# Optimization experiments

Hardware: AMD Instinct MI355X
Metric: run time of the kernel (lower is better)

## Reference

```python
import jax, jax.numpy as jnp
import numpy as np

D_MODEL = 1024
N_HEADS = 16
HEAD_DIM = D_MODEL // N_HEADS
NEG = -10000.0  # module uses -10000, not -inf


def setup_inputs() -> dict:
    key = jax.random.key(0)
    ks = jax.random.split(key, 8)
    B, T = 4, 2048
    q = jax.random.normal(ks[0], (B, T, D_MODEL), dtype=jnp.float32)
    k = jax.random.normal(ks[1], (B, T, D_MODEL), dtype=jnp.float32)
    v = jax.random.normal(ks[2], (B, T, D_MODEL), dtype=jnp.float32)
    attn_mask = jnp.ones((B, T), dtype=jnp.float32)
    # xavier_uniform for square [d, d] weights: limit = sqrt(6/(d+d))
    lim = float(np.sqrt(6.0 / (D_MODEL + D_MODEL)))
    Wq = jax.random.uniform(ks[3], (D_MODEL, D_MODEL), jnp.float32, -lim, lim)
    Wk = jax.random.uniform(ks[4], (D_MODEL, D_MODEL), jnp.float32, -lim, lim)
    Wv = jax.random.uniform(ks[5], (D_MODEL, D_MODEL), jnp.float32, -lim, lim)
    Wo = jax.random.uniform(ks[6], (D_MODEL, D_MODEL), jnp.float32, -lim, lim)
    return {"q": q, "k": k, "v": v, "attn_mask": attn_mask,
            "Wq": Wq, "Wk": Wk, "Wv": Wv, "Wo": Wo, "mask_future": 1}


def _split_heads(x):
    B, T, _ = x.shape
    return x.reshape(B, T, N_HEADS, HEAD_DIM).transpose(0, 2, 1, 3)  # [B,H,T,D]


def reference(q, k, v, attn_mask, Wq, Wk, Wv, Wo, mask_future):
    # torch Linear: y = x @ W.T  (weights stored [out, in])
    qh = _split_heads(jnp.einsum('btd,ed->bte', q, Wq))
    kh = _split_heads(jnp.einsum('btd,ed->bte', k, Wk))
    vh = _split_heads(jnp.einsum('btd,ed->bte', v, Wv))
    L, S = qh.shape[-2], kh.shape[-2]
    # dual scale: each of q and k scaled by 1/d**0.25
    scale = 1.0 / jnp.sqrt(jnp.sqrt(jnp.float32(HEAD_DIM)))
    scores = jnp.einsum('bhld,bhsd->bhls', qh * scale, kh * scale)
    if mask_future:
        causal_bias = jnp.triu(jnp.full((L, S), NEG, dtype=scores.dtype), k=1)
        scores = scores + causal_bias
    # padding mask: attn_mask [B, S] -> broadcast [B,1,1,S]; 0 entries -> -10000
    pad = attn_mask[:, None, None, :]
    scores = jnp.where(pad == 0, jnp.asarray(NEG, scores.dtype), scores)
    probs = jax.nn.softmax(scores, axis=-1)  # dropout p=0.0 -> identity
    ctx = jnp.einsum('bhls,bhsd->bhld', probs, vh)
    B = ctx.shape[0]
    ctx = ctx.transpose(0, 2, 1, 3).reshape(B, L, D_MODEL)
    return jnp.einsum('btd,ed->bte', ctx, Wo)
```

## Files before the change

kernel.cpp:

```cpp
#include <hip/hip_runtime.h>

typedef unsigned short u16;
typedef __attribute__((ext_vector_type(8))) _Float16 f16x8;
typedef __attribute__((ext_vector_type(2))) __fp16 fp16v2;
typedef __attribute__((ext_vector_type(4))) float f32x4;
typedef __attribute__((ext_vector_type(16))) float f32x16;

#define T_SEQ 2048
#define NH 16
#define DH 64
#define DM 1024
#define NEG2 (-14426.95f)
#define QS2 (0.42466089f)

__device__ __forceinline__ unsigned pk2(float a, float b) {
  union { fp16v2 v; unsigned u; } c;
  c.v = __builtin_amdgcn_cvt_pkrtz(a, b);
  return c.u;
}
__device__ __forceinline__ u16 f2h(float a) {
  union { _Float16 h; u16 u; } c; c.h = (_Float16)a; return c.u;
}

__device__ __forceinline__ void async_load16(const void* g, void* l) {
  __builtin_amdgcn_global_load_lds(
      (const __attribute__((address_space(1))) unsigned int*)(g),
      (__attribute__((address_space(3))) unsigned int*)(l), 16, 0, 0);
}

__global__ __launch_bounds__(256) void convert_all(
    const float* __restrict__ q, const float* __restrict__ k, const float* __restrict__ v,
    const float* __restrict__ Wq, const float* __restrict__ Wk, const float* __restrict__ Wv,
    const float* __restrict__ Wo, u16* __restrict__ xb, u16* __restrict__ wb) {
  int blk = blockIdx.x;
  const float* src; u16* dst;
  if (blk < 12288) {
    int s = blk >> 12;
    src = (s == 0) ? q : (s == 1) ? k : v;
    dst = xb + (size_t)s * 8388608u;
    blk &= 4095;
  } else {
    int s = (blk - 12288) >> 9;
    src = (s == 0) ? Wq : (s == 1) ? Wk : (s == 2) ? Wv : Wo;
    dst = wb + (size_t)s * 1048576u;
    blk = (blk - 12288) & 511;
  }
  size_t base = (size_t)blk * 2048 + (size_t)threadIdx.x * 8;
  float4 a = *(const float4*)(src + base);
  float4 b2 = *(const float4*)(src + base + 4);
  uint4 st;
  st.x = pk2(a.x, a.y); st.y = pk2(a.z, a.w);
  st.z = pk2(b2.x, b2.y); st.w = pk2(b2.z, b2.w);
  *(uint4*)(dst + base) = st;
}

__global__ __launch_bounds__(512) void gemm_qkv(const u16* __restrict__ A,
                                                const u16* __restrict__ Wqb,
                                                const u16* __restrict__ Wkb,
                                                const u16* __restrict__ Wvb,
                                                u16* __restrict__ Qh, u16* __restrict__ Kh,
                                                u16* __restrict__ VTh) {
  __shared__ char lds[147456];
  const int tid = threadIdx.x;
  const int wid = tid >> 6, lane = tid & 63;
  const int l32 = lane & 31, lh = lane >> 5;
  const int m0 = blockIdx.x * 256;
  const int n0 = blockIdx.y * 128;
  const int which = n0 >> 10;
  const int n0l = n0 & 1023;
  const u16* As = A + (size_t)which * 8388608u;
  const u16* Bw = (which == 0) ? Wqb : (which == 1) ? Wkb : Wvb;
  f32x16 acc[2][2] = {};

  const u16* gsrc[6]; int ldso[6];
#pragma unroll
  for (int u = 0; u < 6; ++u) {
    int c = wid * 6 + u;
    ldso[u] = c * 1024;
    if (c < 32)
      gsrc[u] = As + (size_t)(m0 + (c >> 2) * 32 + l32) * 1024 + (c & 3) * 16 + lh * 8;
    else {
      int cw = c - 32;
      gsrc[u] = Bw + (size_t)(n0l + (cw >> 2) * 32 + l32) * 1024 + (cw & 3) * 16 + lh * 8;
    }
  }

  const int rOff = (which < 2) ? 32768 : 0;
  const int cOff = 32768 - rOff;
  const int rgo = (which < 2) ? ((wid & 1) * 2) : ((wid >> 1) * 2);
  const int cgo = (which < 2) ? ((wid >> 1) * 2) : ((wid & 1) * 2);

#pragma unroll
  for (int u = 0; u < 6; ++u) async_load16(gsrc[u] + 0 * 64, lds + 0 * 49152 + ldso[u]);
#pragma unroll
  for (int u = 0; u < 6; ++u) async_load16(gsrc[u] + 1 * 64, lds + 1 * 49152 + ldso[u]);
  asm volatile("s_waitcnt vmcnt(6)" ::: "memory");
  __builtin_amdgcn_s_barrier();
  asm volatile("" ::: "memory");

  int slotc = 0, slotn = 2;
  for (int kt = 0; kt < 16; ++kt) {
    char* bufc = lds + slotc * 49152;
    char* bufn = lds + slotn * 49152;
    const char* rb = bufc + rOff;
    const char* cb = bufc + cOff;
    f16x8 a0[4], a1[4], b0[4], b1[4];
#pragma unroll
    for (int k = 0; k < 4; ++k) {
      a0[k] = *(const f16x8*)(rb + ((rgo + 0) * 4 + k) * 1024 + lane * 16);
      b0[k] = *(const f16x8*)(cb + ((cgo + 0) * 4 + k) * 1024 + lane * 16);
      b1[k] = *(const f16x8*)(cb + ((cgo + 1) * 4 + k) * 1024 + lane * 16);
    }
    if (kt < 14) {
#pragma unroll
      for (int u = 0; u < 3; ++u) async_load16(gsrc[u] + (kt + 2) * 64, bufn + ldso[u]);
    }
    asm volatile("" ::: "memory");
    __builtin_amdgcn_s_barrier();
    asm volatile("s_waitcnt lgkmcnt(0)" ::: "memory");
    __builtin_amdgcn_sched_barrier(0);
    __builtin_amdgcn_s_setprio(1);
#pragma unroll
    for (int k = 0; k < 4; ++k) {
      acc[0][0] = __builtin_amdgcn_mfma_f32_32x32x16_f16(a0[k], b0[k], acc[0][0], 0, 0, 0);
      acc[0][1] = __builtin_amdgcn_mfma_f32_32x32x16_f16(a0[k], b1[k], acc[0][1], 0, 0, 0);
    }
    __builtin_amdgcn_s_setprio(0);
    asm volatile("" ::: "memory");
    __builtin_amdgcn_s_barrier();
#pragma unroll
    for (int k = 0; k < 4; ++k)
      a1[k] = *(const f16x8*)(rb + ((rgo + 1) * 4 + k) * 1024 + lane * 16);
    if (kt < 14) {
#pragma unroll
      for (int u = 3; u < 6; ++u) async_load16(gsrc[u] + (kt + 2) * 64, bufn + ldso[u]);
    }
    if (kt < 14) asm volatile("s_waitcnt vmcnt(6)" ::: "memory");
    else         asm volatile("s_waitcnt vmcnt(0)" ::: "memory");
    asm volatile("" ::: "memory");
    __builtin_amdgcn_s_barrier();
    asm volatile("s_waitcnt lgkmcnt(0)" ::: "memory");
    __builtin_amdgcn_sched_barrier(0);
    __builtin_amdgcn_s_setprio(1);
#pragma unroll
    for (int k = 0; k < 4; ++k) {
      acc[1][0] = __builtin_amdgcn_mfma_f32_32x32x16_f16(a1[k], b0[k], acc[1][0], 0, 0, 0);
      acc[1][1] = __builtin_amdgcn_mfma_f32_32x32x16_f16(a1[k], b1[k], acc[1][1], 0, 0, 0);
    }
    __builtin_amdgcn_s_setprio(0);
    asm volatile("" ::: "memory");
    __builtin_amdgcn_s_barrier();
    slotc = (slotc == 2) ? 0 : slotc + 1;
    slotn = (slotn == 2) ? 0 : slotn + 1;
  }

  const float s = (which < 2) ? QS2 : 1.0f;
  const int b = m0 >> 11, t0 = m0 & 2047, h0 = n0l >> 6;
  __syncthreads();
  if (which < 2) {
#pragma unroll
    for (int i = 0; i < 2; ++i)
#pragma unroll
      for (int j = 0; j < 2; ++j) {
        int colb = (wid >> 1) * 64 + j * 32 + l32;
        int rowb = (wid & 1) * 64 + i * 32 + 4 * lh;
#pragma unroll
        for (int g = 0; g < 4; ++g) {
          uint2 pv;
          pv.x = pk2(acc[i][j][4 * g + 0] * s, acc[i][j][4 * g + 1] * s);
          pv.y = pk2(acc[i][j][4 * g + 2] * s, acc[i][j][4 * g + 3] * s);
          *(uint2*)(lds + colb * 264 + (rowb + 8 * g) * 2) = pv;
        }
      }
    __syncthreads();
    u16* O = which ? Kh : Qh;
#pragma unroll
    for (int p = 0; p < 8; ++p) {
      int row = p * 32 + (tid >> 4);
      int seg = tid & 15;
      uint4 val = *(const uint4*)(lds + row * 264 + seg * 16);
      int hl = seg >> 3, dh0 = (seg & 7) * 8;
      *(uint4*)(O + (((size_t)(b * NH + h0 + hl) * T_SEQ + t0 + row) << 6) + dh0) = val;
    }
  } else {
#pragma unroll
    for (int i = 0; i < 2; ++i)
#pragma unroll
      for (int j = 0; j < 2; ++j) {
        int colb = (wid & 1) * 64 + j * 32 + l32;
        int rowb = (wid >> 1) * 64 + i * 32 + 4 * lh;
#pragma unroll
        for (int g = 0; g < 4; ++g) {
          uint2 pv;
          pv.x = pk2(acc[i][j][4 * g + 0], acc[i][j][4 * g + 1]);
          pv.y = pk2(acc[i][j][4 * g + 2], acc[i][j][4 * g + 3]);
          *(uint2*)(lds + colb * 520 + (rowb + 8 * g) * 2) = pv;
        }
      }
    __syncthreads();
#pragma unroll
    for (int p = 0; p < 8; ++p) {
      int row = p * 16 + (tid >> 5);
      int seg = tid & 31;
      uint4 val = *(const uint4*)(lds + row * 520 + seg * 16);
      int h = h0 + (row >> 6), dh = row & 63;
      *(uint4*)(VTh + (((size_t)(b * NH + h) * DH + dh) << 11) + t0 + seg * 8) = val;
    }
  }
}

__global__ __launch_bounds__(512) void gemm_out(const u16* __restrict__ A,
                                                const u16* __restrict__ Bw,
                                                float* __restrict__ O) {
  __shared__ char lds[147456];
  const int tid = threadIdx.x;
  const int wid = tid >> 6, lane = tid & 63;
  const int l32 = lane & 31, lh = lane >> 5;
  const int m0 = blockIdx.x * 256, n0 = blockIdx.y * 128;
  f32x16 acc[2][2] = {};

  const u16* gsrc[6]; int ldso[6];
#pragma unroll
  for (int u = 0; u < 6; ++u) {
    int c = wid * 6 + u;
    ldso[u] = c * 1024;
    if (c < 32)
      gsrc[u] = A + (size_t)(m0 + (c >> 2) * 32 + l32) * 1024 + (c & 3) * 16 + lh * 8;
    else {
      int cw = c - 32;
      gsrc[u] = Bw + (size_t)(n0 + (cw >> 2) * 32 + l32) * 1024 + (cw & 3) * 16 + lh * 8;
    }
  }
  const int rgo = (wid >> 1) * 2, cgo = (wid & 1) * 2;

#pragma unroll
  for (int u = 0; u < 6; ++u) async_load16(gsrc[u] + 0 * 64, lds + 0 * 49152 + ldso[u]);
#pragma unroll
  for (int u = 0; u < 6; ++u) async_load16(gsrc[u] + 1 * 64, lds + 1 * 49152 + ldso[u]);
  asm volatile("s_waitcnt vmcnt(6)" ::: "memory");
  __builtin_amdgcn_s_barrier();
  asm volatile("" ::: "memory");

  int slotc = 0, slotn = 2;
  for (int kt = 0; kt < 16; ++kt) {
    char* bufc = lds + slotc * 49152;
    char* bufn = lds + slotn * 49152;
    const char* rb = bufc;
    const char* cb = bufc + 32768;
    f16x8 a0[4], a1[4], b0[4], b1[4];
#pragma unroll
    for (int k = 0; k < 4; ++k) {
      a0[k] = *(const f16x8*)(rb + ((rgo + 0) * 4 + k) * 1024 + lane * 16);
      b0[k] = *(const f16x8*)(cb + ((cgo + 0) * 4 + k) * 1024 + lane * 16);
      b1[k] = *(const f16x8*)(cb + ((cgo + 1) * 4 + k) * 1024 + lane * 16);
    }
    if (kt < 14) {
#pragma unroll
      for (int u = 0; u < 3; ++u) async_load16(gsrc[u] + (kt + 2) * 64, bufn + ldso[u]);
    }
    asm volatile("" ::: "memory");
    __builtin_amdgcn_s_barrier();
    asm volatile("s_waitcnt lgkmcnt(0)" ::: "memory");
    __builtin_amdgcn_sched_barrier(0);
    __builtin_amdgcn_s_setprio(1);
#pragma unroll
    for (int k = 0; k < 4; ++k) {
      acc[0][0] = __builtin_amdgcn_mfma_f32_32x32x16_f16(a0[k], b0[k], acc[0][0], 0, 0, 0);
      acc[0][1] = __builtin_amdgcn_mfma_f32_32x32x16_f16(a0[k], b1[k], acc[0][1], 0, 0, 0);
    }
    __builtin_amdgcn_s_setprio(0);
    asm volatile("" ::: "memory");
    __builtin_amdgcn_s_barrier();
#pragma unroll
    for (int k = 0; k < 4; ++k)
      a1[k] = *(const f16x8*)(rb + ((rgo + 1) * 4 + k) * 1024 + lane * 16);
    if (kt < 14) {
#pragma unroll
      for (int u = 3; u < 6; ++u) async_load16(gsrc[u] + (kt + 2) * 64, bufn + ldso[u]);
    }
    if (kt < 14) asm volatile("s_waitcnt vmcnt(6)" ::: "memory");
    else         asm volatile("s_waitcnt vmcnt(0)" ::: "memory");
    asm volatile("" ::: "memory");
    __builtin_amdgcn_s_barrier();
    asm volatile("s_waitcnt lgkmcnt(0)" ::: "memory");
    __builtin_amdgcn_sched_barrier(0);
    __builtin_amdgcn_s_setprio(1);
#pragma unroll
    for (int k = 0; k < 4; ++k) {
      acc[1][0] = __builtin_amdgcn_mfma_f32_32x32x16_f16(a1[k], b0[k], acc[1][0], 0, 0, 0);
      acc[1][1] = __builtin_amdgcn_mfma_f32_32x32x16_f16(a1[k], b1[k], acc[1][1], 0, 0, 0);
    }
    __builtin_amdgcn_s_setprio(0);
    asm volatile("" ::: "memory");
    __builtin_amdgcn_s_barrier();
    slotc = (slotc == 2) ? 0 : slotc + 1;
    slotn = (slotn == 2) ? 0 : slotn + 1;
  }
#pragma unroll
  for (int i = 0; i < 2; ++i)
#pragma unroll
    for (int j = 0; j < 2; ++j) {
      int col = n0 + (wid & 1) * 64 + j * 32 + l32;
      int rowb = m0 + (wid >> 1) * 64 + i * 32 + 4 * lh;
#pragma unroll
      for (int g = 0; g < 4; ++g)
#pragma unroll
        for (int rr = 0; rr < 4; ++rr)
          O[(size_t)(rowb + 8 * g + rr) * 1024 + col] = acc[i][j][4 * g + rr];
    }
}

__global__ __launch_bounds__(512) void attn_kernel(const u16* __restrict__ Qh,
                                                   const u16* __restrict__ Kh,
                                                   const u16* __restrict__ VTh,
                                                   const float* __restrict__ attn_mask,
                                                   const int* __restrict__ mfp,
                                                   u16* __restrict__ ctx) {
  __shared__ char kls[2][8192];
  __shared__ char vls[2][8192];
  __shared__ char pls[8][2048];
  __shared__ int mzf;

  const int tid = threadIdx.x;
  const int wid = tid >> 6, lane = tid & 63;
  const int lm = lane & 15, lq = lane >> 4;
  const int bid = blockIdx.x;
  const int bh_i = bid & 63;
  const int qt = 15 - (bid >> 6);
  const int b = bh_i >> 4, h = bh_i & 15;
  const int mf = *mfp;
  const size_t bh = (size_t)(b * NH + h);
  const u16* Qbh = Qh + bh * T_SEQ * DH;
  const u16* Kbh = Kh + bh * T_SEQ * DH;
  const u16* VTbh = VTh + bh * DH * T_SEQ;
  const float* amb = attn_mask + (size_t)b * T_SEQ;

  f16x8 onev;
#pragma unroll
  for (int i = 0; i < 8; ++i) onev[i] = (_Float16)1.0f;

  if (tid == 0) mzf = 0;
  __syncthreads();
  {
    int az = 0;
    for (int i = tid; i < T_SEQ; i += 512) az |= (amb[i] == 0.0f);
    if (az) mzf = 1;
  }
  __syncthreads();
  const int maskzero = mzf;

  const int qw = qt * 128 + wid * 16;
  f16x8 qf[2];
  qf[0] = *(const f16x8*)(Qbh + (size_t)(qw + lm) * DH + lq * 8);
  qf[1] = *(const f16x8*)(Qbh + (size_t)(qw + lm) * DH + 32 + lq * 8);

  f32x4 acc[4] = {};
  f32x4 accs = {};
  float mprev = -1e30f;

  const int nch = mf ? (qt + 1) * 2 : 32;
  {
    async_load16(Kbh + (size_t)((wid >> 1) * 16 + lm) * DH + (wid & 1) * 32 + lq * 8,
                 kls[0] + wid * 1024);
    async_load16(VTbh + (size_t)((wid >> 1) * 16 + lm) * T_SEQ + (wid & 1) * 32 + lq * 8,
                 vls[0] + wid * 1024);
  }
  for (int c = 0; c < nch; ++c) {
    const int s0 = c * 64;
    asm volatile("s_waitcnt vmcnt(0)" ::: "memory");
    __builtin_amdgcn_s_barrier();
    asm volatile("" ::: "memory");
    if (c + 1 < nch) {
      const int s1 = s0 + 64;
      async_load16(Kbh + (size_t)(s1 + (wid >> 1) * 16 + lm) * DH + (wid & 1) * 32 + lq * 8,
                   kls[(c + 1) & 1] + wid * 1024);
      async_load16(VTbh + (size_t)((wid >> 1) * 16 + lm) * T_SEQ + s1 + (wid & 1) * 32 + lq * 8,
                   vls[(c + 1) & 1] + wid * 1024);
    }
    const char* kcur = kls[c & 1];
    const char* vcur = vls[c & 1];

    f32x4 sc[4];
    for (int st = 0; st < 4; ++st) {
      f32x4 z = {0.f, 0.f, 0.f, 0.f};
      sc[st] = z;
      for (int kk = 0; kk < 2; ++kk) {
        f16x8 kf = *(const f16x8*)(kcur + ((st * 2 + kk) * 64 + lane) * 16);
        sc[st] = __builtin_amdgcn_mfma_f32_16x16x32_f16(kf, qf[kk], sc[st], 0, 0, 0);
      }
    }
    if (maskzero) {
      for (int st = 0; st < 4; ++st) {
        f32x4 mb = *(const f32x4*)(amb + s0 + st * 16 + lq * 4);
        for (int r = 0; r < 4; ++r)
          if (mb[r] == 0.0f) sc[st][r] += NEG2;
      }
    }
    if (mf && (s0 + 64 > qw)) {
      int qg = qw + lm;
      for (int st = 0; st < 4; ++st)
        for (int r = 0; r < 4; ++r)
          if (s0 + st * 16 + lq * 4 + r > qg) sc[st][r] = NEG2;
    }
    float u0 = fmaxf(fmaxf(sc[0][0], sc[0][1]), sc[0][2]);
    float u1 = fmaxf(fmaxf(sc[0][3], sc[1][0]), sc[1][1]);
    float u2 = fmaxf(fmaxf(sc[1][2], sc[1][3]), sc[2][0]);
    float u3 = fmaxf(fmaxf(sc[2][1], sc[2][2]), sc[2][3]);
    float u4 = fmaxf(fmaxf(sc[3][0], sc[3][1]), sc[3][2]);
    float mx = fmaxf(fmaxf(fmaxf(u0, u1), u2), fmaxf(fmaxf(u3, u4), sc[3][3]));
    mx = fmaxf(mx, __shfl_xor(mx, 16));
    mx = fmaxf(mx, __shfl_xor(mx, 32));
    if (__ballot(mx > mprev + 8.0f) != 0ull) {
      float mn2 = fmaxf(mprev, mx);
      float alpha = exp2f(mprev - mn2);
      for (int r = 0; r < 4; ++r) {
        float ar = __shfl(alpha, lq * 4 + r);
        for (int nt = 0; nt < 4; ++nt) acc[nt][r] *= ar;
        accs[r] *= ar;
      }
      mprev = mn2;
    }
    for (int st = 0; st < 4; ++st)
      for (int r = 0; r < 4; ++r)
        sc[st][r] = exp2f(sc[st][r] - mprev);
    {
      char* pw = pls[wid];
      for (int st = 0; st < 4; ++st) {
        int kk = st >> 1;
        int lqp = (st & 1) * 2 + (lq >> 1);
        uint2 pv;
        pv.x = pk2(sc[st][0], sc[st][1]);
        pv.y = pk2(sc[st][2], sc[st][3]);
        *(uint2*)(pw + kk * 1024 + (lqp * 16 + lm) * 16 + (lq & 1) * 8) = pv;
      }
    }
    asm volatile("s_waitcnt lgkmcnt(0)" ::: "memory");
    for (int kk = 0; kk < 2; ++kk) {
      f16x8 pf = *(const f16x8*)(pls[wid] + kk * 1024 + lane * 16);
      for (int nt = 0; nt < 4; ++nt) {
        f16x8 vf = *(const f16x8*)(vcur + ((nt * 2 + kk) * 64 + lane) * 16);
        acc[nt] = __builtin_amdgcn_mfma_f32_16x16x32_f16(pf, vf, acc[nt], 0, 0, 0);
      }
      accs = __builtin_amdgcn_mfma_f32_16x16x32_f16(pf, onev, accs, 0, 0, 0);
    }
  }
  for (int r = 0; r < 4; ++r) {
    float ir = 1.0f / accs[r];
    int t = qw + lq * 4 + r;
    for (int nt = 0; nt < 4; ++nt)
      ctx[((size_t)(b * T_SEQ + t) * DM) + h * DH + nt * 16 + lm] = f2h(acc[nt][r] * ir);
  }
}

extern "C" void kernel_launch(void* const* d_in, const int* in_sizes, int n_in,
                              void* d_out, int out_size, void* d_ws, size_t ws_size,
                              hipStream_t stream) {
  const float* q = (const float*)d_in[0];
  const float* k = (const float*)d_in[1];
  const float* v = (const float*)d_in[2];
  const float* attn_mask = (const float*)d_in[3];
  const float* Wq = (const float*)d_in[4];
  const float* Wk = (const float*)d_in[5];
  const float* Wv = (const float*)d_in[6];
  const float* Wo = (const float*)d_in[7];
  const int* mf = (const int*)d_in[8];

  u16* ws = (u16*)d_ws;
  u16* qb  = ws;
  u16* wqb = ws + 3u * 8388608u;
  u16* wkb = wqb + 1048576u;
  u16* wvb = wkb + 1048576u;
  u16* wob = wvb + 1048576u;
  u16* Qh  = wob + 1048576u;
  u16* Kh  = Qh + 8388608u;
  u16* VTh = Kh + 8388608u;
  u16* ctxb = ws;

  convert_all<<<14336, 256, 0, stream>>>(q, k, v, Wq, Wk, Wv, Wo, qb, wqb);

  dim3 gq(32, 24);
  gemm_qkv<<<gq, 512, 0, stream>>>(qb, wqb, wkb, wvb, Qh, Kh, VTh);

  attn_kernel<<<1024, 512, 0, stream>>>(Qh, Kh, VTh, attn_mask, mf, ctxb);

  dim3 gg(32, 8);
  gemm_out<<<gg, 512, 0, stream>>>(ctxb, wob, (float*)d_out);
}
```

Before: 337.8 us.

## Halve GEMM K-tile and LDS footprint with single-barrier triple-buffered pipeline

```diff
diff --git a/kernel.cpp b/kernel.cpp
--- a/kernel.cpp
+++ b/kernel.cpp
@@ -60,7 +60,7 @@
                                                 const u16* __restrict__ Wvb,
                                                 u16* __restrict__ Qh, u16* __restrict__ Kh,
                                                 u16* __restrict__ VTh) {
-  __shared__ char lds[147456];
+  __shared__ char lds[73728];
   const int tid = threadIdx.x;
   const int wid = tid >> 6, lane = tid & 63;
   const int l32 = lane & 31, lh = lane >> 5;
@@ -72,84 +72,67 @@
   const u16* Bw = (which == 0) ? Wqb : (which == 1) ? Wkb : Wvb;
   f32x16 acc[2][2] = {};
 
-  const u16* gsrc[6]; int ldso[6];
-#pragma unroll
-  for (int u = 0; u < 6; ++u) {
-    int c = wid * 6 + u;
+  const u16* gsrc[3]; int ldso[3];
+#pragma unroll
+  for (int u = 0; u < 3; ++u) {
+    int c = wid * 3 + u;
     ldso[u] = c * 1024;
-    if (c < 32)
-      gsrc[u] = As + (size_t)(m0 + (c >> 2) * 32 + l32) * 1024 + (c & 3) * 16 + lh * 8;
+    if (c < 16)
+      gsrc[u] = As + (size_t)(m0 + (c >> 1) * 32 + l32) * 1024 + (c & 1) * 16 + lh * 8;
     else {
-      int cw = c - 32;
-      gsrc[u] = Bw + (size_t)(n0l + (cw >> 2) * 32 + l32) * 1024 + (cw & 3) * 16 + lh * 8;
-    }
-  }
-
-  const int rOff = (which < 2) ? 32768 : 0;
-  const int cOff = 32768 - rOff;
+      int cw = c - 16;
+      gsrc[u] = Bw + (size_t)(n0l + (cw >> 1) * 32 + l32) * 1024 + (cw & 1) * 16 + lh * 8;
+    }
+  }
+
+  const int rOff = (which < 2) ? 16384 : 0;
+  const int cOff = 16384 - rOff;
   const int rgo = (which < 2) ? ((wid & 1) * 2) : ((wid >> 1) * 2);
   const int cgo = (which < 2) ? ((wid >> 1) * 2) : ((wid & 1) * 2);
 
 #pragma unroll
-  for (int u = 0; u < 6; ++u) async_load16(gsrc[u] + 0 * 64, lds + 0 * 49152 + ldso[u]);
-#pragma unroll
-  for (int u = 0; u < 6; ++u) async_load16(gsrc[u] + 1 * 64, lds + 1 * 49152 + ldso[u]);
-  asm volatile("s_waitcnt vmcnt(6)" ::: "memory");
-  __builtin_amdgcn_s_barrier();
-  asm volatile("" ::: "memory");
+  for (int u = 0; u < 3; ++u) async_load16(gsrc[u] + 0 * 32, lds + 0 * 24576 + ldso[u]);
+#pragma unroll
+  for (int u = 0; u < 3; ++u) async_load16(gsrc[u] + 1 * 32, lds + 1 * 24576 + ldso[u]);
 
   int slotc = 0, slotn = 2;
-  for (int kt = 0; kt < 16; ++kt) {
-    char* bufc = lds + slotc * 49152;
-    char* bufn = lds + slotn * 49152;
+  for (int kt = 0; kt < 32; ++kt) {
+    if (kt < 31) asm volatile("s_waitcnt vmcnt(3)" ::: "memory");
+    else         asm volatile("s_waitcnt vmcnt(0)" ::: "memory");
+    __builtin_amdgcn_s_barrier();
+    asm volatile("" ::: "memory");
+    char* bufc = lds + slotc * 24576;
+    if (kt < 30) {
+      char* bufn = lds + slotn * 24576;
+      int ko = (kt + 2) * 32;
+#pragma unroll
+      for (int u = 0; u < 3; ++u) async_load16(gsrc[u] + ko, bufn + ldso[u]);
+    }
     const char* rb = bufc + rOff;
     const char* cb = bufc + cOff;
-    f16x8 a0[4], a1[4], b0[4], b1[4];
-#pragma unroll
-    for (int k = 0; k < 4; ++k) {
-      a0[k] = *(const f16x8*)(rb + ((rgo + 0) * 4 + k) * 1024 + lane * 16);
-      b0[k] = *(const f16x8*)(cb + ((cgo + 0) * 4 + k) * 1024 + lane * 16);
-      b1[k] = *(const f16x8*)(cb + ((cgo + 1) * 4 + k) * 1024 + lane * 16);
-    }
-    if (kt < 14) {
-#pragma unroll
-      for (int u = 0; u < 3; ++u) async_load16(gsrc[u] + (kt + 2) * 64, bufn + ldso[u]);
-    }
-    asm volatile("" ::: "memory");
-    __builtin_amdgcn_s_barrier();
-    asm volatile("s_waitcnt lgkmcnt(0)" ::: "memory");
-    __builtin_amdgcn_sched_barrier(0);
+    f16x8 r0[2], c0[2], r1[2], c1[2];
+#pragma unroll
+    for (int i = 0; i < 2; ++i) {
+      r0[i] = *(const f16x8*)(rb + ((rgo + i) * 2 + 0) * 1024 + lane * 16);
+      c0[i] = *(const f16x8*)(cb + ((cgo + i) * 2 + 0) * 1024 + lane * 16);
+    }
+#pragma unroll
+    for (int i = 0; i < 2; ++i) {
+      r1[i] = *(const f16x8*)(rb + ((rgo + i) * 2 + 1) * 1024 + lane * 16);
+      c1[i] = *(const f16x8*)(cb + ((cgo + i) * 2 + 1) * 1024 + lane * 16);
+    }
     __builtin_amdgcn_s_setprio(1);
 #pragma unroll
-    for (int k = 0; k < 4; ++k) {
-      acc[0][0] = __builtin_amdgcn_mfma_f32_32x32x16_f16(a0[k], b0[k], acc[0][0], 0, 0, 0);
-      acc[0][1] = __builtin_amdgcn_mfma_f32_32x32x16_f16(a0[k], b1[k], acc[0][1], 0, 0, 0);
-    }
+    for (int i = 0; i < 2; ++i)
+#pragma unroll
+      for (int j = 0; j < 2; ++j)
+        acc[i][j] = __builtin_amdgcn_mfma_f32_32x32x16_f16(r0[i], c0[j], acc[i][j], 0, 0, 0);
+#pragma unroll
+    for (int i = 0; i < 2; ++i)
+#pragma unroll
+      for (int j = 0; j < 2; ++j)
+        acc[i][j] = __builtin_amdgcn_mfma_f32_32x32x16_f16(r1[i], c1[j], acc[i][j], 0, 0, 0);
     __builtin_amdgcn_s_setprio(0);
-    asm volatile("" ::: "memory");
-    __builtin_amdgcn_s_barrier();
-#pragma unroll
-    for (int k = 0; k < 4; ++k)
-      a1[k] = *(const f16x8*)(rb + ((rgo + 1) * 4 + k) * 1024 + lane * 16);
-    if (kt < 14) {
-#pragma unroll
-      for (int u = 3; u < 6; ++u) async_load16(gsrc[u] + (kt + 2) * 64, bufn + ldso[u]);
-    }
-    if (kt < 14) asm volatile("s_waitcnt vmcnt(6)" ::: "memory");
-    else         asm volatile("s_waitcnt vmcnt(0)" ::: "memory");
-    asm volatile("" ::: "memory");
-    __builtin_amdgcn_s_barrier();
-    asm volatile("s_waitcnt lgkmcnt(0)" ::: "memory");
-    __builtin_amdgcn_sched_barrier(0);
-    __builtin_amdgcn_s_setprio(1);
-#pragma unroll
-    for (int k = 0; k < 4; ++k) {
-      acc[1][0] = __builtin_amdgcn_mfma_f32_32x32x16_f16(a1[k], b0[k], acc[1][0], 0, 0, 0);
-      acc[1][1] = __builtin_amdgcn_mfma_f32_32x32x16_f16(a1[k], b1[k], acc[1][1], 0, 0, 0);
-    }
-    __builtin_amdgcn_s_setprio(0);
-    asm volatile("" ::: "memory");
-    __builtin_amdgcn_s_barrier();
     slotc = (slotc == 2) ? 0 : slotc + 1;
     slotn = (slotn == 2) ? 0 : slotn + 1;
   }
@@ -212,87 +195,70 @@
 __global__ __launch_bounds__(512) void gemm_out(const u16* __restrict__ A,
                                                 const u16* __restrict__ Bw,
                                                 float* __restrict__ O) {
-  __shared__ char lds[147456];
+  __shared__ char lds[73728];
   const int tid = threadIdx.x;
   const int wid = tid >> 6, lane = tid & 63;
   const int l32 = lane & 31, lh = lane >> 5;
   const int m0 = blockIdx.x * 256, n0 = blockIdx.y * 128;
   f32x16 acc[2][2] = {};
 
-  const u16* gsrc[6]; int ldso[6];
-#pragma unroll
-  for (int u = 0; u < 6; ++u) {
-    int c = wid * 6 + u;
+  const u16* gsrc[3]; int ldso[3];
+#pragma unroll
+  for (int u = 0; u < 3; ++u) {
+    int c = wid * 3 + u;
     ldso[u] = c * 1024;
-    if (c < 32)
-      gsrc[u] = A + (size_t)(m0 + (c >> 2) * 32 + l32) * 1024 + (c & 3) * 16 + lh * 8;
+    if (c < 16)
+      gsrc[u] = A + (size_t)(m0 + (c >> 1) * 32 + l32) * 1024 + (c & 1) * 16 + lh * 8;
     else {
-      int cw = c - 32;
-      gsrc[u] = Bw + (size_t)(n0 + (cw >> 2) * 32 + l32) * 1024 + (cw & 3) * 16 + lh * 8;
+      int cw = c - 16;
+      gsrc[u] = Bw + (size_t)(n0 + (cw >> 1) * 32 + l32) * 1024 + (cw & 1) * 16 + lh * 8;
     }
   }
   const int rgo = (wid >> 1) * 2, cgo = (wid & 1) * 2;
 
 #pragma unroll
-  for (int u = 0; u < 6; ++u) async_load16(gsrc[u] + 0 * 64, lds + 0 * 49152 + ldso[u]);
-#pragma unroll
-  for (int u = 0; u < 6; ++u) async_load16(gsrc[u] + 1 * 64, lds + 1 * 49152 + ldso[u]);
-  asm volatile("s_waitcnt vmcnt(6)" ::: "memory");
-  __builtin_amdgcn_s_barrier();
-  asm volatile("" ::: "memory");
+  for (int u = 0; u < 3; ++u) async_load16(gsrc[u] + 0 * 32, lds + 0 * 24576 + ldso[u]);
+#pragma unroll
+  for (int u = 0; u < 3; ++u) async_load16(gsrc[u] + 1 * 32, lds + 1 * 24576 + ldso[u]);
 
   int slotc = 0, slotn = 2;
-  for (int kt = 0; kt < 16; ++kt) {
-    char* bufc = lds + slotc * 49152;
-    char* bufn = lds + slotn * 49152;
+  for (int kt = 0; kt < 32; ++kt) {
+    if (kt < 31) asm volatile("s_waitcnt vmcnt(3)" ::: "memory");
+    else         asm volatile("s_waitcnt vmcnt(0)" ::: "memory");
+    __builtin_amdgcn_s_barrier();
+    asm volatile("" ::: "memory");
+    char* bufc = lds + slotc * 24576;
+    if (kt < 30) {
+      char* bufn = lds + slotn * 24576;
+      int ko = (kt + 2) * 32;
+#pragma unroll
+      for (int u = 0; u < 3; ++u) async_load16(gsrc[u] + ko, bufn + ldso[u]);
+    }
     const char* rb = bufc;
-    const char* cb = bufc + 32768;
-    f16x8 a0[4], a1[4], b0[4], b1[4];
-#pragma unroll
-    for (int k = 0; k < 4; ++k) {
-      a0[k] = *(const f16x8*)(rb + ((rgo + 0) * 4 + k) * 1024 + lane * 16);
-      b0[k] = *(const f16x8*)(cb + ((cgo + 0) * 4 + k) * 1024 + lane * 16);
-      b1[k] = *(const f16x8*)(cb + ((cgo + 1) * 4 + k) * 1024 + lane * 16);
-    }
-    if (kt < 14) {
-#pragma unroll
-      for (int u = 0; u < 3; ++u) async_load16(gsrc[u] + (kt + 2) * 64, bufn + ldso[u]);
-    }
-    asm volatile("" ::: "memory");
-    __builtin_amdgcn_s_barrier();
-    asm volatile("s_waitcnt lgkmcnt(0)" ::: "memory");
-    __builtin_amdgcn_sched_barrier(0);
+    const char* cb = bufc + 16384;
+    f16x8 r0[2], c0[2], r1[2], c1[2];
+#pragma unroll
+    for (int i = 0; i < 2; ++i) {
+      r0[i] = *(const f16x8*)(rb + ((rgo + i) * 2 + 0) * 1024 + lane * 16);
+      c0[i] = *(const f16x8*)(cb + ((cgo + i) * 2 + 0) * 1024 + lane * 16);
+    }
+#pragma unroll
+    for (int i = 0; i < 2; ++i) {
+      r1[i] = *(const f16x8*)(rb + ((rgo + i) * 2 + 1) * 1024 + lane * 16);
+      c1[i] = *(const f16x8*)(cb + ((cgo + i) * 2 + 1) * 1024 + lane * 16);
+    }
     __builtin_amdgcn_s_setprio(1);
 #pragma unroll
-    for (int k = 0; k < 4; ++k) {
-      acc[0][0] = __builtin_amdgcn_mfma_f32_32x32x16_f16(a0[k], b0[k], acc[0][0], 0, 0, 0);
-      acc[0][1] = __builtin_amdgcn_mfma_f32_32x32x16_f16(a0[k], b1[k], acc[0][1], 0, 0, 0);
-    }
+    for (int i = 0; i < 2; ++i)
+#pragma unroll
+      for (int j = 0; j < 2; ++j)
+        acc[i][j] = __builtin_amdgcn_mfma_f32_32x32x16_f16(r0[i], c0[j], acc[i][j], 0, 0, 0);
+#pragma unroll
+    for (int i = 0; i < 2; ++i)
+#pragma unroll
+      for (int j = 0; j < 2; ++j)
+        acc[i][j] = __builtin_amdgcn_mfma_f32_32x32x16_f16(r1[i], c1[j], acc[i][j], 0, 0, 0);
     __builtin_amdgcn_s_setprio(0);
-    asm volatile("" ::: "memory");
-    __builtin_amdgcn_s_barrier();
-#pragma unroll
-    for (int k = 0; k < 4; ++k)
-      a1[k] = *(const f16x8*)(rb + ((rgo + 1) * 4 + k) * 1024 + lane * 16);
-    if (kt < 14) {
-#pragma unroll
-      for (int u = 3; u < 6; ++u) async_load16(gsrc[u] + (kt + 2) * 64, bufn + ldso[u]);
-    }
-    if (kt < 14) asm volatile("s_waitcnt vmcnt(6)" ::: "memory");
-    else         asm volatile("s_waitcnt vmcnt(0)" ::: "memory");
-    asm volatile("" ::: "memory");
-    __builtin_amdgcn_s_barrier();
-    asm volatile("s_waitcnt lgkmcnt(0)" ::: "memory");
-    __builtin_amdgcn_sched_barrier(0);
-    __builtin_amdgcn_s_setprio(1);
-#pragma unroll
-    for (int k = 0; k < 4; ++k) {
-      acc[1][0] = __builtin_amdgcn_mfma_f32_32x32x16_f16(a1[k], b0[k], acc[1][0], 0, 0, 0);
-      acc[1][1] = __builtin_amdgcn_mfma_f32_32x32x16_f16(a1[k], b1[k], acc[1][1], 0, 0, 0);
-    }
-    __builtin_amdgcn_s_setprio(0);
-    asm volatile("" ::: "memory");
-    __builtin_amdgcn_s_barrier();
     slotc = (slotc == 2) ? 0 : slotc + 1;
     slotn = (slotn == 2) ? 0 : slotn + 1;
   }
```

New measurement: 331.6 us. No clear change (-1.8%).
